# Performance work log

Hardware: AMD Instinct MI355X
Metric: run time of the kernel (lower is better)

Reference implementation:

```python
import jax, jax.numpy as jnp
import numpy as np

D_MODEL = 1024
N_HEADS = 16
HEAD_DIM = D_MODEL // N_HEADS  # 64


def setup_inputs() -> dict:
    key = jax.random.key(0)
    k1, k2, k3 = jax.random.split(key, 3)
    B, T = 2, 2048
    x = jax.random.normal(k1, (B, T, D_MODEL), dtype=jnp.float32)
    # nn.Linear(d, 3d) weight applied as x @ W (stored transposed vs torch)
    W_qkv = jax.random.normal(k2, (D_MODEL, 3 * D_MODEL), dtype=jnp.float32) / np.sqrt(D_MODEL)
    W_proj = jax.random.normal(k3, (D_MODEL, D_MODEL), dtype=jnp.float32) / np.sqrt(D_MODEL)
    return {"x": x, "W_qkv": W_qkv, "W_proj": W_proj}


def reference(x, W_qkv, W_proj):
    B, T, D = x.shape
    qkv = x @ W_qkv  # [B, T, 3D]
    qkv = qkv.reshape(B, T, 3, N_HEADS, HEAD_DIM)
    qkv = jnp.transpose(qkv, (2, 0, 3, 1, 4))  # [3, B, H, T, hd]
    q, k, v = qkv[0], qkv[1], qkv[2]
    # muP 'readout' attn_score: scale by 1/head_dim (instead of 1/sqrt(head_dim))
    attn = jnp.einsum('bhqd,bhkd->bhqk', q, k) / HEAD_DIM  # [B, H, T, T]
    attn = jax.nn.softmax(attn, axis=-1)
    out = jnp.einsum('bhqk,bhkd->bhqd', attn, v)  # [B, H, T, hd]
    out = jnp.transpose(out, (0, 2, 1, 3)).reshape(B, T, D)
    return out @ W_proj
```

## Files before the change

kernel.cpp:

```cpp
#include <hip/hip_runtime.h>
#include <hip/hip_bf16.h>
#include <hip/hip_fp16.h>
#include <stdint.h>

#define B_    2
#define T_    2048
#define DM    1024
#define NH    16
#define HD    64
#define M_    (B_ * T_)
#define N_QKV (3 * DM)

typedef __attribute__((ext_vector_type(8))) __bf16 bf16x8;
typedef __attribute__((ext_vector_type(4))) float  v4f;
typedef __attribute__((ext_vector_type(2))) __fp16 fp16x2;
typedef __attribute__((ext_vector_type(4))) _Float16 h4;
typedef __attribute__((ext_vector_type(8))) _Float16 h8;
typedef __hip_bfloat16 bf16;

#define EXP_SC 0.022542110013890053f

__device__ __forceinline__ void gld_lds16(const void* g, void* l) {
  __builtin_amdgcn_global_load_lds(
      (const __attribute__((address_space(1))) void*)(g),
      (__attribute__((address_space(3))) void*)(l), 16, 0, 0);
}


__global__ void cast_f32_bf16(const float* __restrict__ in, bf16* __restrict__ out) {
  int i = (blockIdx.x * 256 + threadIdx.x) * 4;
  float4 v = *(const float4*)(in + i);
  union { bf16 h[4]; ushort4 u; } r;
  r.h[0] = __float2bfloat16(v.x); r.h[1] = __float2bfloat16(v.y);
  r.h[2] = __float2bfloat16(v.z); r.h[3] = __float2bfloat16(v.w);
  *(ushort4*)(out + i) = r.u;
}

__global__ void transpose_cast(const float* __restrict__ in, bf16* __restrict__ out,
                               int R, int C) {
  __shared__ float tile[32][33];
  int c0 = blockIdx.x * 32, r0 = blockIdx.y * 32;
  int tx = threadIdx.x, ty = threadIdx.y;
  #pragma unroll
  for (int i = ty; i < 32; i += 8)
    tile[i][tx] = in[(size_t)(r0 + i) * C + c0 + tx];
  __syncthreads();
  #pragma unroll
  for (int i = ty; i < 32; i += 8)
    out[(size_t)(c0 + i) * R + r0 + tx] = __float2bfloat16(tile[tx][i]);
}

__global__ __launch_bounds__(256) void transpose_v(
    const _Float16* __restrict__ in, _Float16* __restrict__ out) {
  __shared__ _Float16 tl[64][72];
  const int tid = threadIdx.x, bh = blockIdx.y, t0 = blockIdx.x * 64;
  const size_t ib = (size_t)bh * T_ * HD, ob = (size_t)bh * HD * T_;
  #pragma unroll
  for (int i = 0; i < 2; ++i) {
    int flat = (i * 256 + tid) * 8;
    int r = flat >> 6, c = flat & 63;
    *(uint4*)(&tl[r][c]) = *(const uint4*)(in + ib + (size_t)(t0 + r) * HD + c);
  }
  __syncthreads();
  int d = tid >> 2, c0 = (tid & 3) * 16;
  #pragma unroll
  for (int j = 0; j < 16; j += 8) {
    union { _Float16 h[8]; uint4 u; } pk;
    #pragma unroll
    for (int k2 = 0; k2 < 8; ++k2) pk.h[k2] = tl[c0 + j + k2][d];
    *(uint4*)(out + ob + (size_t)d * T_ + t0 + c0 + j) = pk.u;
  }
}

template <int MODE>
__global__ __launch_bounds__(256) void gemm_bt(
    const bf16* __restrict__ A, const bf16* __restrict__ BT,
    float* __restrict__ Cf, bf16* __restrict__ qb, bf16* __restrict__ kb,
    _Float16* __restrict__ vb, int M, int N, int K) {
  __shared__ bf16 As[128 * 64];
  __shared__ bf16 Bs[128 * 64];
  const int tid = threadIdx.x;
  const int l = tid & 63, w = tid >> 6;
  const int wm = w >> 1, wn = w & 1;
  const int m0 = blockIdx.y * 128, n0 = blockIdx.x * 128;
  const int fr = l & 15;
  const int lg = l >> 4;

  v4f acc[4][4] = {};

  for (int kt = 0; kt < K; kt += 64) {
    __syncthreads();
    #pragma unroll
    for (int i = 0; i < 4; ++i) {
      int p = i * 256 + tid;
      int row = p >> 3, g = (p & 7) ^ (row & 7);
      gld_lds16(A + (size_t)(m0 + row) * K + kt + g * 8, As + p * 8);
      gld_lds16(BT + (size_t)(n0 + row) * K + kt + g * 8, Bs + p * 8);
    }
    __syncthreads();
    #pragma unroll
    for (int kk = 0; kk < 64; kk += 32) {
      const int gl = (kk >> 3) + lg;
      bf16x8 af[4], bfr[4];
      #pragma unroll
      for (int i = 0; i < 4; ++i) {
        int row = wm * 64 + i * 16 + fr;
        af[i] = *(const bf16x8*)(As + row * 64 + (gl ^ (fr & 7)) * 8);
      }
      #pragma unroll
      for (int i = 0; i < 4; ++i) {
        int row = wn * 64 + i * 16 + fr;
        bfr[i] = *(const bf16x8*)(Bs + row * 64 + (gl ^ (fr & 7)) * 8);
      }
      #pragma unroll
      for (int mi = 0; mi < 4; ++mi)
        #pragma unroll
        for (int ni = 0; ni < 4; ++ni)
          acc[mi][ni] = __builtin_amdgcn_mfma_f32_16x16x32_bf16(
              af[mi], bfr[ni], acc[mi][ni], 0, 0, 0);
    }
  }

  #pragma unroll
  for (int mi = 0; mi < 4; ++mi) {
    #pragma unroll
    for (int ni = 0; ni < 4; ++ni) {
      #pragma unroll
      for (int r = 0; r < 4; ++r) {
        int gm = m0 + wm * 64 + mi * 16 + (l >> 4) * 4 + r;
        int gn = n0 + wn * 64 + ni * 16 + (l & 15);
        float v = acc[mi][ni][r];
        if constexpr (MODE == 0) {
          Cf[(size_t)gm * N + gn] = v;
        } else {
          int b = gm >> 11, t = gm & 2047;
          int s = gn >> 10, h = (gn >> 6) & 15, d = gn & 63;
          size_t bh = (size_t)(b * NH + h);
          if (s == 0)      qb[(bh * T_ + t) * HD + d] = __float2bfloat16(v);
          else if (s == 1) kb[(bh * T_ + t) * HD + d] = __float2bfloat16(v);
          else             vb[(bh * T_ + t) * HD + d] = (_Float16)v;
        }
      }
    }
  }
}

__global__ __launch_bounds__(256) void gemm_bt_n64(
    const bf16* __restrict__ A, const bf16* __restrict__ BT,
    float* __restrict__ Cf, int M, int N, int K) {
  __shared__ bf16 As[128 * 64];
  __shared__ bf16 Bs[64 * 64];
  const int tid = threadIdx.x;
  const int l = tid & 63, w = tid >> 6;
  const int wm = w >> 1, wn = w & 1;
  const int m0 = blockIdx.y * 128, n0 = blockIdx.x * 64;
  const int fr = l & 15;
  const int lg = l >> 4;

  v4f acc[4][2] = {};

  for (int kt = 0; kt < K; kt += 64) {
    __syncthreads();
    #pragma unroll
    for (int i = 0; i < 4; ++i) {
      int p = i * 256 + tid;
      int row = p >> 3, g = (p & 7) ^ (row & 7);
      gld_lds16(A + (size_t)(m0 + row) * K + kt + g * 8, As + p * 8);
    }
    #pragma unroll
    for (int i = 0; i < 2; ++i) {
      int p = i * 256 + tid;
      int row = p >> 3, g = (p & 7) ^ (row & 7);
      gld_lds16(BT + (size_t)(n0 + row) * K + kt + g * 8, Bs + p * 8);
    }
    __syncthreads();
    #pragma unroll
    for (int kk = 0; kk < 64; kk += 32) {
      const int gl = (kk >> 3) + lg;
      bf16x8 af[4], bfr[2];
      #pragma unroll
      for (int i = 0; i < 4; ++i) {
        int row = wm * 64 + i * 16 + fr;
        af[i] = *(const bf16x8*)(As + row * 64 + (gl ^ (fr & 7)) * 8);
      }
      #pragma unroll
      for (int i = 0; i < 2; ++i) {
        int row = wn * 32 + i * 16 + fr;
        bfr[i] = *(const bf16x8*)(Bs + row * 64 + (gl ^ (fr & 7)) * 8);
      }
      #pragma unroll
      for (int mi = 0; mi < 4; ++mi)
        #pragma unroll
        for (int ni = 0; ni < 2; ++ni)
          acc[mi][ni] = __builtin_amdgcn_mfma_f32_16x16x32_bf16(
              af[mi], bfr[ni], acc[mi][ni], 0, 0, 0);
    }
  }

  #pragma unroll
  for (int mi = 0; mi < 4; ++mi)
    #pragma unroll
    for (int ni = 0; ni < 2; ++ni)
      #pragma unroll
      for (int r = 0; r < 4; ++r) {
        int gm = m0 + wm * 64 + mi * 16 + (l >> 4) * 4 + r;
        int gn = n0 + wn * 32 + ni * 16 + (l & 15);
        Cf[(size_t)gm * N + gn] = acc[mi][ni][r];
      }
}

__global__ __launch_bounds__(256) void flash_attn(
    const bf16* __restrict__ Qg, const bf16* __restrict__ Kg,
    const _Float16* __restrict__ VTg, bf16* __restrict__ Og) {
  __shared__ char smem[53248];
  bf16*     Ks = (bf16*)smem;
  _Float16* Vs = (_Float16*)(smem + 16384);
  _Float16 (*Ps)[40] = (_Float16(*)[40])(smem + 32768);
  float*    Obuf = (float*)smem;
  float*    Lbuf = (float*)(smem + 34816);

  const int tid = threadIdx.x, l = tid & 63, w = tid >> 6;
  const int qh = w & 1, kh = w >> 1;
  const int fr = l & 15, fk = (l >> 4) * 8, g4 = (l >> 4) * 4, lg = l >> 4;
  const int bh = blockIdx.y, qt = blockIdx.x;
  const int q0 = qt * 128 + qh * 64;
  const size_t base  = (size_t)bh * T_ * HD;
  const size_t baseV = (size_t)bh * HD * T_;
  _Float16 (*Pw)[40] = Ps + w * 64;

  bf16x8 qB[4][2];
  #pragma unroll
  for (int qf = 0; qf < 4; ++qf)
    #pragma unroll
    for (int kki = 0; kki < 2; ++kki)
      qB[qf][kki] = *(const bf16x8*)(
          Qg + base + (size_t)(q0 + qf * 16 + fr) * HD + kki * 32 + fk);

  h8 ones;
  #pragma unroll
  for (int j = 0; j < 8; ++j) ones[j] = (_Float16)1.0f;

  v4f o[4][4] = {};
  v4f lacc[4] = {};

  for (int kt = 0; kt < T_; kt += 128) {
    __syncthreads();
    #pragma unroll
    for (int i = 0; i < 4; ++i) {
      int p = i * 256 + tid;
      int krow = p >> 3, kg = (p & 7) ^ (krow & 7);
      gld_lds16(Kg + base + (size_t)(kt + krow) * HD + kg * 8, Ks + p * 8);
      int vrow = p >> 4, vg = (p & 15) ^ (vrow & 15);
      gld_lds16(VTg + baseV + (size_t)vrow * T_ + kt + vg * 8, Vs + p * 8);
    }
    __syncthreads();

    #pragma unroll
    for (int c = 0; c < 2; ++c) {
      const int kkg = kh * 2 + c;
      #pragma unroll
      for (int hf = 0; hf < 2; ++hf) {
        const int kf = kkg * 2 + hf;
        v4f st[4] = {};
        #pragma unroll
        for (int kki = 0; kki < 2; ++kki) {
          int row = kf * 16 + fr;
          bf16x8 ak = *(const bf16x8*)(
              Ks + row * 64 + ((kki * 4 + lg) ^ (fr & 7)) * 8);
          #pragma unroll
          for (int qf = 0; qf < 4; ++qf)
            st[qf] = __builtin_amdgcn_mfma_f32_16x16x32_bf16(
                ak, qB[qf][kki], st[qf], 0, 0, 0);
        }
        #pragma unroll
        for (int qf = 0; qf < 4; ++qf) {
          union { fp16x2 p2[2]; h4 p4; } u;
          u.p2[0] = __builtin_amdgcn_cvt_pkrtz(
              __builtin_amdgcn_exp2f(st[qf][0] * EXP_SC),
              __builtin_amdgcn_exp2f(st[qf][1] * EXP_SC));
          u.p2[1] = __builtin_amdgcn_cvt_pkrtz(
              __builtin_amdgcn_exp2f(st[qf][2] * EXP_SC),
              __builtin_amdgcn_exp2f(st[qf][3] * EXP_SC));
          *(h4*)(&Pw[qf * 16 + fr][hf * 16 + g4]) = u.p4;
        }
      }
      h8 ap[4], bv[4];
      #pragma unroll
      for (int qf = 0; qf < 4; ++qf)
        ap[qf] = *(const h8*)(&Pw[qf * 16 + fr][fk]);
      #pragma unroll
      for (int nf = 0; nf < 4; ++nf) {
        int row = nf * 16 + fr;
        bv[nf] = *(const h8*)(Vs + row * 128 + ((kkg * 4 + lg) ^ fr) * 8);
      }
      #pragma unroll
      for (int qf = 0; qf < 4; ++qf) {
        lacc[qf] = __builtin_amdgcn_mfma_f32_16x16x32_f16(
            ap[qf], ones, lacc[qf], 0, 0, 0);
        #pragma unroll
        for (int nf = 0; nf < 4; ++nf)
          o[qf][nf] = __builtin_amdgcn_mfma_f32_16x16x32_f16(
              ap[qf], bv[nf], o[qf][nf], 0, 0, 0);
      }
    }
  }

  __syncthreads();
  if (w >= 2) {
    #pragma unroll
    for (int qf = 0; qf < 4; ++qf)
      #pragma unroll
      for (int r = 0; r < 4; ++r) {
        int row = qf * 16 + g4 + r;
        #pragma unroll
        for (int nf = 0; nf < 4; ++nf)
          Obuf[(qh * 64 + row) * 68 + nf * 16 + fr] = o[qf][nf][r];
        if (fr == 0) Lbuf[qh * 64 + row] = lacc[qf][r];
      }
  }
  __syncthreads();
  if (w < 2) {
    int b = bh >> 4, h = bh & 15;
    #pragma unroll
    for (int qf = 0; qf < 4; ++qf) {
      #pragma unroll
      for (int r = 0; r < 4; ++r) {
        int row = qf * 16 + g4 + r;
        float inv = 1.f / (lacc[qf][r] + Lbuf[qh * 64 + row]);
        int t = q0 + row;
        #pragma unroll
        for (int nf = 0; nf < 4; ++nf) {
          float val = o[qf][nf][r] + Obuf[(qh * 64 + row) * 68 + nf * 16 + fr];
          Og[((size_t)(b * T_ + t)) * DM + h * HD + nf * 16 + fr] =
              __float2bfloat16(val * inv);
        }
      }
    }
  }
}

extern "C" void kernel_launch(void* const* d_in, const int* in_sizes, int n_in,
                              void* d_out, int out_size, void* d_ws, size_t ws_size,
                              hipStream_t stream) {
  const float* x     = (const float*)d_in[0];
  const float* Wqkv  = (const float*)d_in[1];
  const float* Wproj = (const float*)d_in[2];
  float* out = (float*)d_out;
  char* ws = (char*)d_ws;

  bf16*     Xb     = (bf16*)(ws);
  bf16*     WqkvT  = (bf16*)(ws + (size_t)( 8u << 20));
  bf16*     WprojT = (bf16*)(ws + (size_t)(14u << 20));
  bf16*     Qb     = (bf16*)(ws + (size_t)(16u << 20));
  bf16*     Kb     = (bf16*)(ws + (size_t)(24u << 20));
  _Float16* VTh    = (_Float16*)(ws + (size_t)(32u << 20));
  _Float16* Vh     = (_Float16*)(ws + (size_t)(40u << 20));
  bf16*     Ab     = (bf16*)(ws + (size_t)(40u << 20));

  cast_f32_bf16<<<(M_ * DM) / 1024, 256, 0, stream>>>(x, Xb);
  transpose_cast<<<dim3(N_QKV / 32, DM / 32), dim3(32, 8), 0, stream>>>(Wqkv, WqkvT, DM, N_QKV);
  transpose_cast<<<dim3(DM / 32, DM / 32), dim3(32, 8), 0, stream>>>(Wproj, WprojT, DM, DM);

  gemm_bt<1><<<dim3(N_QKV / 128, M_ / 128), 256, 0, stream>>>(
      Xb, WqkvT, nullptr, Qb, Kb, Vh, M_, N_QKV, DM);

  transpose_v<<<dim3(T_ / 64, B_ * NH), 256, 0, stream>>>(Vh, VTh);

  flash_attn<<<dim3(T_ / 128, B_ * NH), 256, 0, stream>>>(Qb, Kb, VTh, Ab);

  gemm_bt_n64<<<dim3(DM / 64, M_ / 128), 256, 0, stream>>>(
      Ab, WprojT, out, M_, DM, DM);
}
```

Before: 196.5 us.

## Double-buffer K/V tiles in flash attention and fold softmax scale into Q

Replaces the single-buffered 128-key loop, which loaded and then fully synchronized, with a double-buffered 64-key pipeline. The next tile's K and V^T are prefetched into the alternate LDS buffer via global_load_lds while the current one is computed, using explicit vmcnt waits and raw s_barrier. The exp2 scale factor is folded into Q when the QKV GEMM writes it, which removes a multiply per score element. The risks are more barriers per key and correctness that relies on hand-coded waitcnt encodings. Bf16 rounding of the pre-scaled Q also changes precision slightly.

```diff
diff --git a/kernel.cpp b/kernel.cpp
--- a/kernel.cpp
+++ b/kernel.cpp
@@ -19,6 +19,9 @@
 typedef __hip_bfloat16 bf16;
 
 #define EXP_SC 0.022542110013890053f
+
+#define WAITCNT_VM4 0x0F74
+#define WAITCNT_VM0 0x0F70
 
 __device__ __forceinline__ void gld_lds16(const void* g, void* l) {
   __builtin_amdgcn_global_load_lds(
@@ -136,7 +139,7 @@
           int b = gm >> 11, t = gm & 2047;
           int s = gn >> 10, h = (gn >> 6) & 15, d = gn & 63;
           size_t bh = (size_t)(b * NH + h);
-          if (s == 0)      qb[(bh * T_ + t) * HD + d] = __float2bfloat16(v);
+          if (s == 0)      qb[(bh * T_ + t) * HD + d] = __float2bfloat16(v * EXP_SC);
           else if (s == 1) kb[(bh * T_ + t) * HD + d] = __float2bfloat16(v);
           else             vb[(bh * T_ + t) * HD + d] = (_Float16)v;
         }
@@ -213,8 +216,8 @@
     const bf16* __restrict__ Qg, const bf16* __restrict__ Kg,
     const _Float16* __restrict__ VTg, bf16* __restrict__ Og) {
   __shared__ char smem[53248];
-  bf16*     Ks = (bf16*)smem;
-  _Float16* Vs = (_Float16*)(smem + 16384);
+  bf16*     KsB = (bf16*)smem;
+  _Float16* VsB = (_Float16*)(smem + 16384);
   _Float16 (*Ps)[40] = (_Float16(*)[40])(smem + 32768);
   float*    Obuf = (float*)smem;
   float*    Lbuf = (float*)(smem + 34816);
@@ -243,65 +246,86 @@
   v4f o[4][4] = {};
   v4f lacc[4] = {};
 
-  for (int kt = 0; kt < T_; kt += 128) {
-    __syncthreads();
-    #pragma unroll
-    for (int i = 0; i < 4; ++i) {
-      int p = i * 256 + tid;
-      int krow = p >> 3, kg = (p & 7) ^ (krow & 7);
-      gld_lds16(Kg + base + (size_t)(kt + krow) * HD + kg * 8, Ks + p * 8);
-      int vrow = p >> 4, vg = (p & 15) ^ (vrow & 15);
-      gld_lds16(VTg + baseV + (size_t)vrow * T_ + kt + vg * 8, Vs + p * 8);
-    }
-    __syncthreads();
-
-    #pragma unroll
-    for (int c = 0; c < 2; ++c) {
-      const int kkg = kh * 2 + c;
-      #pragma unroll
-      for (int hf = 0; hf < 2; ++hf) {
-        const int kf = kkg * 2 + hf;
-        v4f st[4] = {};
-        #pragma unroll
-        for (int kki = 0; kki < 2; ++kki) {
-          int row = kf * 16 + fr;
-          bf16x8 ak = *(const bf16x8*)(
-              Ks + row * 64 + ((kki * 4 + lg) ^ (fr & 7)) * 8);
-          #pragma unroll
-          for (int qf = 0; qf < 4; ++qf)
-            st[qf] = __builtin_amdgcn_mfma_f32_16x16x32_bf16(
-                ak, qB[qf][kki], st[qf], 0, 0, 0);
-        }
-        #pragma unroll
-        for (int qf = 0; qf < 4; ++qf) {
-          union { fp16x2 p2[2]; h4 p4; } u;
-          u.p2[0] = __builtin_amdgcn_cvt_pkrtz(
-              __builtin_amdgcn_exp2f(st[qf][0] * EXP_SC),
-              __builtin_amdgcn_exp2f(st[qf][1] * EXP_SC));
-          u.p2[1] = __builtin_amdgcn_cvt_pkrtz(
-              __builtin_amdgcn_exp2f(st[qf][2] * EXP_SC),
-              __builtin_amdgcn_exp2f(st[qf][3] * EXP_SC));
-          *(h4*)(&Pw[qf * 16 + fr][hf * 16 + g4]) = u.p4;
-        }
-      }
-      h8 ap[4], bv[4];
-      #pragma unroll
-      for (int qf = 0; qf < 4; ++qf)
-        ap[qf] = *(const h8*)(&Pw[qf * 16 + fr][fk]);
-      #pragma unroll
-      for (int nf = 0; nf < 4; ++nf) {
-        int row = nf * 16 + fr;
-        bv[nf] = *(const h8*)(Vs + row * 128 + ((kkg * 4 + lg) ^ fr) * 8);
+  #pragma unroll
+  for (int i = 0; i < 2; ++i) {
+    int p = i * 256 + tid;
+    int row = p >> 3, g = (p & 7) ^ (row & 7);
+    gld_lds16(Kg + base + (size_t)row * HD + g * 8, KsB + p * 8);
+    gld_lds16(VTg + baseV + (size_t)row * T_ + g * 8, VsB + p * 8);
+  }
+
+  for (int t = 0; t < 32; ++t) {
+    const int cur = t & 1;
+    bf16*     Kc = KsB + cur * 4096;
+    _Float16* Vc = VsB + cur * 4096;
+
+    __asm__ volatile("" ::: "memory");
+    __builtin_amdgcn_s_barrier();
+    __asm__ volatile("" ::: "memory");
+
+    if (t < 31) {
+      const int ktn = (t + 1) * 64;
+      bf16*     Kn = KsB + (1 - cur) * 4096;
+      _Float16* Vn = VsB + (1 - cur) * 4096;
+      #pragma unroll
+      for (int i = 0; i < 2; ++i) {
+        int p = i * 256 + tid;
+        int row = p >> 3, g = (p & 7) ^ (row & 7);
+        gld_lds16(Kg + base + (size_t)(ktn + row) * HD + g * 8, Kn + p * 8);
+        gld_lds16(VTg + baseV + (size_t)row * T_ + ktn + g * 8, Vn + p * 8);
+      }
+      __asm__ volatile("" ::: "memory");
+      __builtin_amdgcn_s_waitcnt(WAITCNT_VM4);
+    } else {
+      __asm__ volatile("" ::: "memory");
+      __builtin_amdgcn_s_waitcnt(WAITCNT_VM0);
+    }
+    __asm__ volatile("" ::: "memory");
+    __builtin_amdgcn_s_barrier();
+    __asm__ volatile("" ::: "memory");
+
+    #pragma unroll
+    for (int kf = 0; kf < 2; ++kf) {
+      const int krow = kh * 32 + kf * 16 + fr;
+      v4f st[4] = {};
+      #pragma unroll
+      for (int kki = 0; kki < 2; ++kki) {
+        bf16x8 ak = *(const bf16x8*)(
+            Kc + krow * 64 + ((kki * 4 + lg) ^ (fr & 7)) * 8);
+        #pragma unroll
+        for (int qf = 0; qf < 4; ++qf)
+          st[qf] = __builtin_amdgcn_mfma_f32_16x16x32_bf16(
+              ak, qB[qf][kki], st[qf], 0, 0, 0);
       }
       #pragma unroll
       for (int qf = 0; qf < 4; ++qf) {
-        lacc[qf] = __builtin_amdgcn_mfma_f32_16x16x32_f16(
-            ap[qf], ones, lacc[qf], 0, 0, 0);
-        #pragma unroll
-        for (int nf = 0; nf < 4; ++nf)
-          o[qf][nf] = __builtin_amdgcn_mfma_f32_16x16x32_f16(
-              ap[qf], bv[nf], o[qf][nf], 0, 0, 0);
-      }
+        union { fp16x2 p2[2]; h4 p4; } u;
+        u.p2[0] = __builtin_amdgcn_cvt_pkrtz(
+            __builtin_amdgcn_exp2f(st[qf][0]),
+            __builtin_amdgcn_exp2f(st[qf][1]));
+        u.p2[1] = __builtin_amdgcn_cvt_pkrtz(
+            __builtin_amdgcn_exp2f(st[qf][2]),
+            __builtin_amdgcn_exp2f(st[qf][3]));
+        *(h4*)(&Pw[qf * 16 + fr][kf * 16 + g4]) = u.p4;
+      }
+    }
+    h8 ap[4], bv[4];
+    #pragma unroll
+    for (int qf = 0; qf < 4; ++qf)
+      ap[qf] = *(const h8*)(&Pw[qf * 16 + fr][fk]);
+    #pragma unroll
+    for (int nf = 0; nf < 4; ++nf) {
+      int row = nf * 16 + fr;
+      bv[nf] = *(const h8*)(Vc + row * 64 + ((kh * 4 + lg) ^ (fr & 7)) * 8);
+    }
+    #pragma unroll
+    for (int qf = 0; qf < 4; ++qf) {
+      lacc[qf] = __builtin_amdgcn_mfma_f32_16x16x32_f16(
+          ap[qf], ones, lacc[qf], 0, 0, 0);
+      #pragma unroll
+      for (int nf = 0; nf < 4; ++nf)
+        o[qf][nf] = __builtin_amdgcn_mfma_f32_16x16x32_f16(
+            ap[qf], bv[nf], o[qf][nf], 0, 0, 0);
     }
   }
 
```

Result: slower. 201.6 us (+2.6%).
